# Kernel tuning notes

Hardware: AMD Instinct MI355X
Metric: run time of the kernel (lower is better)

Reference implementation:

```python
import jax, jax.numpy as jnp
import numpy as np

B, S, D = 8, 2048, 1024
NEG = -1000000000.0  # float32 masking constant from original code


def setup_inputs() -> dict:
    key = jax.random.key(0)
    kq, kk, kv, km = jax.random.split(key, 4)
    q = jax.random.normal(kq, (B, S, D), dtype=jnp.float32)
    k = jax.random.normal(kk, (B, S, D), dtype=jnp.float32)
    v = jax.random.normal(kv, (B, S, D), dtype=jnp.float32)
    mask = (jax.random.uniform(km, (B, 1, S)) < 0.1).astype(jnp.float32)
    return {"q": q, "k": k, "v": v, "mask": mask}


def reference(q, k, v, mask):
    scale = jnp.asarray(D ** -0.5, dtype=q.dtype)
    # [B,S,S] = q @ k^T, scaled
    logits = jnp.einsum("bqd,bkd->bqk", q, k) * scale
    logits = logits + mask * NEG  # mask broadcasts over query axis
    attn = jax.nn.softmax(logits, axis=-1)
    return jnp.einsum("bqk,bkd->bqd", attn, v)
```

## Files before the change

### kernel.cpp

```cpp
#include <hip/hip_runtime.h>
#include <hip/hip_bf16.h>

#define NB 8
#define SS 2048
#define DDIM 1024

typedef __attribute__((ext_vector_type(8))) short bf16x8;
typedef __attribute__((ext_vector_type(4))) float f32x4;

__device__ inline void gload_lds16(const void* g, void* l) {
  __builtin_amdgcn_global_load_lds(
      (const __attribute__((address_space(1))) void*)g,
      (__attribute__((address_space(3))) void*)l, 16, 0, 0);
}

__device__ inline ushort f2bf(float f) {
  union { float f; unsigned int u; } v;
  v.f = f;
  unsigned int u = v.u;
  unsigned int r = (u + 0x7FFFu + ((u >> 16) & 1u)) >> 16;
  return (ushort)r;
}

__device__ inline unsigned int pack2(float a, float b) {
  return (unsigned int)f2bf(a) | ((unsigned int)f2bf(b) << 16);
}

__global__ void init_zero(float* __restrict__ p, int n) {
  int i = blockIdx.x * 256 + threadIdx.x;
  if (i < n) p[i] = 0.f;
}

__global__ void conv_bf16(const float* __restrict__ in, ushort* __restrict__ out,
                          int n8) {
  int i = blockIdx.x * 256 + threadIdx.x;
  if (i >= n8) return;
  const float4* p = (const float4*)in + (size_t)i * 2;
  float4 a = p[0], b = p[1];
  uint4 o;
  o.x = pack2(a.x, a.y);
  o.y = pack2(a.z, a.w);
  o.z = pack2(b.x, b.y);
  o.w = pack2(b.z, b.w);
  ((uint4*)out)[i] = o;
}

__global__ void conv_transpose_v(const float* __restrict__ V,
                                 ushort* __restrict__ VT) {
  __shared__ ushort tile[64][65];
  const int b = blockIdx.z;
  const int k0 = blockIdx.x * 64;
  const int d0 = blockIdx.y * 64;
  const float* Vb = V + (size_t)b * SS * DDIM;
  ushort* VTb = VT + (size_t)b * DDIM * SS;
  const int t = threadIdx.x;
#pragma unroll
  for (int i = 0; i < 16; i++) {
    int flat = i * 256 + t;
    int r = flat >> 6, c = flat & 63;
    tile[r][c] = f2bf(Vb[(size_t)(k0 + r) * DDIM + d0 + c]);
  }
  __syncthreads();
#pragma unroll
  for (int i = 0; i < 16; i++) {
    int flat = i * 256 + t;
    int r = flat >> 6, c = flat & 63;
    VTb[(size_t)(d0 + r) * SS + k0 + c] = tile[c][r];
  }
}

template <bool EXPEPI, typename OutT>
__global__ void gemm_bt(const ushort* __restrict__ A, const ushort* __restrict__ Bm,
                        OutT* __restrict__ C, const float* __restrict__ maskp,
                        float* __restrict__ rowsum, int M, int N, int K,
                        float alpha) {
  __shared__ ushort lA[128 * 32];
  __shared__ ushort lB[128 * 32];
  const int tid = threadIdx.x;
  const int wave = tid >> 6, lane = tid & 63;
  const int quad = lane >> 4, l16 = lane & 15;
  const int wm = wave >> 1, wn = wave & 1;
  const int b = blockIdx.z;
  const ushort* Ab = A + (size_t)b * M * K;
  const ushort* Bb = Bm + (size_t)b * N * K;
  const int tileM = blockIdx.y * 128, tileN = blockIdx.x * 128;

  f32x4 acc[4][4];
#pragma unroll
  for (int i = 0; i < 4; i++)
#pragma unroll
    for (int j = 0; j < 4; j++) acc[i][j] = (f32x4){0.f, 0.f, 0.f, 0.f};

  for (int k0 = 0; k0 < K; k0 += 32) {
#pragma unroll
    for (int c = 0; c < 2; c++) {
      int flat = (wave * 2 + c) * 1024 + lane * 16;
      int row = flat >> 6, kb = flat & 63;
      gload_lds16((const char*)Ab + ((size_t)(tileM + row) * K + k0) * 2 + kb,
                  (char*)lA + flat);
      gload_lds16((const char*)Bb + ((size_t)(tileN + row) * K + k0) * 2 + kb,
                  (char*)lB + flat);
    }
    asm volatile("s_waitcnt vmcnt(0)" ::: "memory");
    __syncthreads();

    bf16x8 af[4], bfr[4];
#pragma unroll
    for (int mi = 0; mi < 4; mi++)
      af[mi] = *(const bf16x8*)((const char*)lA +
                                ((wm * 64 + mi * 16 + l16) * 32 + quad * 8) * 2);
#pragma unroll
    for (int ni = 0; ni < 4; ni++)
      bfr[ni] = *(const bf16x8*)((const char*)lB +
                                 ((wn * 64 + ni * 16 + l16) * 32 + quad * 8) * 2);
#pragma unroll
    for (int mi = 0; mi < 4; mi++)
#pragma unroll
      for (int ni = 0; ni < 4; ni++)
        acc[mi][ni] = __builtin_amdgcn_mfma_f32_16x16x32_bf16(af[mi], bfr[ni],
                                                              acc[mi][ni], 0, 0, 0);
    __syncthreads();
  }

  OutT* Cb = C + (size_t)b * M * N;
  if (EXPEPI) {
    const float* mb = maskp + (size_t)b * N;
    float mv[4];
#pragma unroll
    for (int ni = 0; ni < 4; ni++)
      mv[ni] = mb[tileN + wn * 64 + ni * 16 + l16] * (-1e9f);
#pragma unroll
    for (int mi = 0; mi < 4; mi++) {
#pragma unroll
      for (int r = 0; r < 4; r++) {
        int row = tileM + wm * 64 + mi * 16 + quad * 4 + r;
        float s = 0.f;
#pragma unroll
        for (int ni = 0; ni < 4; ni++) {
          int col = tileN + wn * 64 + ni * 16 + l16;
          float e = __expf(acc[mi][ni][r] * alpha + mv[ni]);
          ((ushort*)Cb)[(size_t)row * N + col] = f2bf(e);
          s += e;
        }
        s += __shfl_xor(s, 1, 64);
        s += __shfl_xor(s, 2, 64);
        s += __shfl_xor(s, 4, 64);
        s += __shfl_xor(s, 8, 64);
        if (l16 == 0) atomicAdd(&rowsum[(size_t)b * M + row], s);
      }
    }
  } else {
#pragma unroll
    for (int mi = 0; mi < 4; mi++) {
      float inv[4];
#pragma unroll
      for (int r = 0; r < 4; r++) {
        int row = tileM + wm * 64 + mi * 16 + quad * 4 + r;
        inv[r] = 1.0f / rowsum[(size_t)b * M + row];
      }
#pragma unroll
      for (int ni = 0; ni < 4; ni++) {
        int col = tileN + wn * 64 + ni * 16 + l16;
#pragma unroll
        for (int r = 0; r < 4; r++) {
          int row = tileM + wm * 64 + mi * 16 + quad * 4 + r;
          ((float*)Cb)[(size_t)row * N + col] = acc[mi][ni][r] * alpha * inv[r];
        }
      }
    }
  }
}

extern "C" void kernel_launch(void* const* d_in, const int* in_sizes, int n_in,
                              void* d_out, int out_size, void* d_ws, size_t ws_size,
                              hipStream_t stream) {
  const float* q = (const float*)d_in[0];
  const float* k = (const float*)d_in[1];
  const float* v = (const float*)d_in[2];
  const float* mask = (const float*)d_in[3];
  float* out = (float*)d_out;

  const size_t pQ = (size_t)SS * DDIM * 2;
  const size_t pP = (size_t)SS * SS * 2;
  const size_t pR = (size_t)SS * 4;

  int gb = 8;
  while (gb > 1 && (size_t)gb * (3 * pQ + pP + pR) > ws_size) gb >>= 1;

  for (int b0 = 0; b0 < NB; b0 += gb) {
    char* w = (char*)d_ws;
    ushort* qb = (ushort*)w;
    ushort* kb = (ushort*)(w + (size_t)gb * pQ);
    ushort* vtb = (ushort*)(w + (size_t)gb * pQ * 2);
    ushort* Sc = (ushort*)(w + (size_t)gb * pQ * 3);
    float* rowsum = (float*)(w + (size_t)gb * (pQ * 3 + pP));

    const float* qg = q + (size_t)b0 * SS * DDIM;
    const float* kg = k + (size_t)b0 * SS * DDIM;
    const float* vg = v + (size_t)b0 * SS * DDIM;
    const float* mg = mask + (size_t)b0 * SS;
    float* og = out + (size_t)b0 * SS * DDIM;

    const int nrs = gb * SS;
    init_zero<<<(nrs + 255) / 256, 256, 0, stream>>>(rowsum, nrs);
    const int n8 = gb * SS * DDIM / 8;
    conv_bf16<<<n8 / 256, 256, 0, stream>>>(qg, qb, n8);
    conv_bf16<<<n8 / 256, 256, 0, stream>>>(kg, kb, n8);
    conv_transpose_v<<<dim3(SS / 64, DDIM / 64, gb), 256, 0, stream>>>(vg, vtb);
    gemm_bt<true, ushort><<<dim3(SS / 128, SS / 128, gb), 256, 0, stream>>>(
        qb, kb, Sc, mg, rowsum, SS, SS, DDIM, 0.03125f);
    gemm_bt<false, float><<<dim3(DDIM / 128, SS / 128, gb), 256, 0, stream>>>(
        Sc, vtb, og, nullptr, rowsum, SS, DDIM, SS, 1.0f);
  }
}
```

Measured before the change: 412.0 us.

## Double-buffer GEMM K-loop with swizzled LDS, XCD remap, and vectorized conversions

```diff
diff --git a/kernel.cpp b/kernel.cpp
--- a/kernel.cpp
+++ b/kernel.cpp
@@ -31,10 +31,14 @@
   if (i < n) p[i] = 0.f;
 }
 
-__global__ void conv_bf16(const float* __restrict__ in, ushort* __restrict__ out,
-                          int n8) {
+__global__ void conv_bf16_qk(const float* __restrict__ qin,
+                             const float* __restrict__ kin,
+                             ushort* __restrict__ qout,
+                             ushort* __restrict__ kout, int n8) {
   int i = blockIdx.x * 256 + threadIdx.x;
   if (i >= n8) return;
+  const float* in = blockIdx.y ? kin : qin;
+  ushort* out = blockIdx.y ? kout : qout;
   const float4* p = (const float4*)in + (size_t)i * 2;
   float4 a = p[0], b = p[1];
   uint4 o;
@@ -55,71 +59,145 @@
   ushort* VTb = VT + (size_t)b * DDIM * SS;
   const int t = threadIdx.x;
 #pragma unroll
-  for (int i = 0; i < 16; i++) {
-    int flat = i * 256 + t;
-    int r = flat >> 6, c = flat & 63;
-    tile[r][c] = f2bf(Vb[(size_t)(k0 + r) * DDIM + d0 + c]);
+  for (int i = 0; i < 4; i++) {
+    int j = i * 256 + t;
+    int r = j >> 4, cg = j & 15;
+    float4 f = *(const float4*)(Vb + (size_t)(k0 + r) * DDIM + d0 + cg * 4);
+    tile[r][cg * 4 + 0] = f2bf(f.x);
+    tile[r][cg * 4 + 1] = f2bf(f.y);
+    tile[r][cg * 4 + 2] = f2bf(f.z);
+    tile[r][cg * 4 + 3] = f2bf(f.w);
   }
   __syncthreads();
 #pragma unroll
-  for (int i = 0; i < 16; i++) {
-    int flat = i * 256 + t;
-    int r = flat >> 6, c = flat & 63;
-    VTb[(size_t)(d0 + r) * SS + k0 + c] = tile[c][r];
-  }
-}
+  for (int i = 0; i < 2; i++) {
+    int j = i * 256 + t;
+    int r = j >> 3, cg = j & 7;
+    ushort u[8];
+#pragma unroll
+    for (int u8 = 0; u8 < 8; u8++) u[u8] = tile[cg * 8 + u8][r];
+    *(uint4*)(VTb + (size_t)(d0 + r) * SS + k0 + cg * 8) = *(uint4*)u;
+  }
+}
+
+#define MFMA32()                                                              \
+  _Pragma("unroll") for (int ks = 0; ks < 2; ks++)                            \
+  _Pragma("unroll") for (int mi = 0; mi < 4; mi++)                            \
+  _Pragma("unroll") for (int ni = 0; ni < 4; ni++)                            \
+      acc[mi][ni] = __builtin_amdgcn_mfma_f32_16x16x32_bf16(                  \
+          af[mi][ks], bf[ni][ks], acc[mi][ni], 0, 0, 0);
+
+#define VMW(n) asm volatile("s_waitcnt vmcnt(" #n ")" ::: "memory")
+
+#define RD_A(d)                                                               \
+  _Pragma("unroll") for (int mi = 0; mi < 4; mi++) {                          \
+    const char* _p = ldsc + (d) * 32768 + aoff[mi];                           \
+    af[mi][0] = *(const bf16x8*)(_p + koff0);                                 \
+    af[mi][1] = *(const bf16x8*)(_p + koff1);                                 \
+  }
+
+#define RD_B(d)                                                               \
+  _Pragma("unroll") for (int ni = 0; ni < 4; ni++) {                          \
+    const char* _p = ldsc + (d) * 32768 + 16384 + boff[ni];                   \
+    bf[ni][0] = *(const bf16x8*)(_p + koff0);                                 \
+    bf[ni][1] = *(const bf16x8*)(_p + koff1);                                 \
+  }
+
+#define STAGE(dbuf, kt_)                                                      \
+  do {                                                                        \
+    const ushort* _pa = pA + (size_t)(kt_) * 64;                              \
+    const ushort* _pb = pB + (size_t)(kt_) * 64;                              \
+    char* _la = ldsc + (dbuf) * 32768;                                        \
+    char* _lb = _la + 16384;                                                  \
+    gload_lds16(_pa, _la + olb);                                              \
+    gload_lds16(_pa + 8 * K, _la + olb + 1024);                               \
+    gload_lds16(_pa + 16 * K, _la + olb + 2048);                              \
+    gload_lds16(_pa + 24 * K, _la + olb + 3072);                              \
+    gload_lds16(_pb, _lb + olb);                                              \
+    gload_lds16(_pb + 8 * K, _lb + olb + 1024);                               \
+    gload_lds16(_pb + 16 * K, _lb + olb + 2048);                              \
+    gload_lds16(_pb + 24 * K, _lb + olb + 3072);                              \
+  } while (0)
 
 template <bool EXPEPI, typename OutT>
-__global__ void gemm_bt(const ushort* __restrict__ A, const ushort* __restrict__ Bm,
-                        OutT* __restrict__ C, const float* __restrict__ maskp,
-                        float* __restrict__ rowsum, int M, int N, int K,
-                        float alpha) {
-  __shared__ ushort lA[128 * 32];
-  __shared__ ushort lB[128 * 32];
+__global__ __launch_bounds__(256, 2) void gemm_bt(
+    const ushort* __restrict__ A, const ushort* __restrict__ Bm,
+    OutT* __restrict__ C, const float* __restrict__ maskp,
+    float* __restrict__ rowsum, int M, int N, int K, float alpha) {
+  __shared__ __attribute__((aligned(128))) char ldsc[65536];
   const int tid = threadIdx.x;
   const int wave = tid >> 6, lane = tid & 63;
   const int quad = lane >> 4, l16 = lane & 15;
   const int wm = wave >> 1, wn = wave & 1;
-  const int b = blockIdx.z;
+
+  const int gx = gridDim.x, gy = gridDim.y;
+  const int lin = blockIdx.x + gx * (blockIdx.y + gy * blockIdx.z);
+  const int nwg = gx * gy * (int)gridDim.z;
+  const int cpx = nwg >> 3;
+  const int swz = (lin & 7) * cpx + (lin >> 3);
+  const int bz = swz / (gx * gy);
+  const int rem = swz - bz * (gx * gy);
+  const int by = rem / gx;
+  const int bx = rem - by * gx;
+
+  const int b = bz;
   const ushort* Ab = A + (size_t)b * M * K;
   const ushort* Bb = Bm + (size_t)b * N * K;
-  const int tileM = blockIdx.y * 128, tileN = blockIdx.x * 128;
+  const int tileM = by * 128, tileN = bx * 128;
+
+  const int olb = wave * 4096 + lane * 16;
+  const int r0 = wave * 32 + (lane >> 3);
+  const int c8 = (((lane & 7) ^ (r0 & 7)) * 8);
+  const ushort* __restrict__ pA = Ab + (size_t)(tileM + r0) * K + c8;
+  const ushort* __restrict__ pB = Bb + (size_t)(tileN + r0) * K + c8;
+
+  const int x7 = lane & 7;
+  const int koff0 = ((quad) ^ x7) * 16;
+  const int koff1 = ((4 + quad) ^ x7) * 16;
+  int aoff[4], boff[4];
+#pragma unroll
+  for (int mi = 0; mi < 4; mi++) aoff[mi] = (wm * 64 + mi * 16 + l16) * 128;
+#pragma unroll
+  for (int ni = 0; ni < 4; ni++) boff[ni] = (wn * 64 + ni * 16 + l16) * 128;
 
   f32x4 acc[4][4];
 #pragma unroll
-  for (int i = 0; i < 4; i++)
-#pragma unroll
-    for (int j = 0; j < 4; j++) acc[i][j] = (f32x4){0.f, 0.f, 0.f, 0.f};
-
-  for (int k0 = 0; k0 < K; k0 += 32) {
-#pragma unroll
-    for (int c = 0; c < 2; c++) {
-      int flat = (wave * 2 + c) * 1024 + lane * 16;
-      int row = flat >> 6, kb = flat & 63;
-      gload_lds16((const char*)Ab + ((size_t)(tileM + row) * K + k0) * 2 + kb,
-                  (char*)lA + flat);
-      gload_lds16((const char*)Bb + ((size_t)(tileN + row) * K + k0) * 2 + kb,
-                  (char*)lB + flat);
-    }
-    asm volatile("s_waitcnt vmcnt(0)" ::: "memory");
-    __syncthreads();
-
-    bf16x8 af[4], bfr[4];
-#pragma unroll
-    for (int mi = 0; mi < 4; mi++)
-      af[mi] = *(const bf16x8*)((const char*)lA +
-                                ((wm * 64 + mi * 16 + l16) * 32 + quad * 8) * 2);
-#pragma unroll
-    for (int ni = 0; ni < 4; ni++)
-      bfr[ni] = *(const bf16x8*)((const char*)lB +
-                                 ((wn * 64 + ni * 16 + l16) * 32 + quad * 8) * 2);
-#pragma unroll
-    for (int mi = 0; mi < 4; mi++)
-#pragma unroll
-      for (int ni = 0; ni < 4; ni++)
-        acc[mi][ni] = __builtin_amdgcn_mfma_f32_16x16x32_bf16(af[mi], bfr[ni],
-                                                              acc[mi][ni], 0, 0, 0);
-    __syncthreads();
+  for (int mi = 0; mi < 4; mi++)
+#pragma unroll
+    for (int ni = 0; ni < 4; ni++) acc[mi][ni] = (f32x4){0.f, 0.f, 0.f, 0.f};
+
+  bf16x8 af[4][2], bf[4][2];
+  const int NKT = K >> 6;
+
+  STAGE(0, 0);
+
+  for (int kt = 0; kt < NKT - 1; ++kt) {
+    const int d = kt & 1, dn = d ^ 1;
+    STAGE(dn, kt + 1);
+    VMW(8);
+    __builtin_amdgcn_s_barrier();
+    RD_A(d);
+    RD_B(d);
+    asm volatile("s_waitcnt lgkmcnt(0)" ::: "memory");
+    __builtin_amdgcn_sched_barrier(0);
+    __builtin_amdgcn_s_setprio(1);
+    MFMA32();
+    __builtin_amdgcn_s_setprio(0);
+    __builtin_amdgcn_sched_barrier(0);
+    __builtin_amdgcn_s_barrier();
+  }
+  {
+    const int d = (NKT - 1) & 1;
+    VMW(0);
+    __builtin_amdgcn_s_barrier();
+    RD_A(d);
+    RD_B(d);
+    asm volatile("s_waitcnt lgkmcnt(0)" ::: "memory");
+    __builtin_amdgcn_sched_barrier(0);
+    __builtin_amdgcn_s_setprio(1);
+    MFMA32();
+    __builtin_amdgcn_s_setprio(0);
+    __builtin_amdgcn_sched_barrier(0);
   }
 
   OutT* Cb = C + (size_t)b * M * N;
@@ -132,13 +210,13 @@
 #pragma unroll
     for (int mi = 0; mi < 4; mi++) {
 #pragma unroll
-      for (int r = 0; r < 4; r++) {
-        int row = tileM + wm * 64 + mi * 16 + quad * 4 + r;
+      for (int rr = 0; rr < 4; rr++) {
+        const int row = tileM + wm * 64 + mi * 16 + quad * 4 + rr;
         float s = 0.f;
 #pragma unroll
         for (int ni = 0; ni < 4; ni++) {
-          int col = tileN + wn * 64 + ni * 16 + l16;
-          float e = __expf(acc[mi][ni][r] * alpha + mv[ni]);
+          const int col = tileN + wn * 64 + ni * 16 + l16;
+          float e = __expf(acc[mi][ni][rr] * alpha + mv[ni]);
           ((ushort*)Cb)[(size_t)row * N + col] = f2bf(e);
           s += e;
         }
@@ -154,17 +232,17 @@
     for (int mi = 0; mi < 4; mi++) {
       float inv[4];
 #pragma unroll
-      for (int r = 0; r < 4; r++) {
-        int row = tileM + wm * 64 + mi * 16 + quad * 4 + r;
-        inv[r] = 1.0f / rowsum[(size_t)b * M + row];
+      for (int rr = 0; rr < 4; rr++) {
+        const int row = tileM + wm * 64 + mi * 16 + quad * 4 + rr;
+        inv[rr] = 1.0f / rowsum[(size_t)b * M + row];
       }
 #pragma unroll
       for (int ni = 0; ni < 4; ni++) {
-        int col = tileN + wn * 64 + ni * 16 + l16;
-#pragma unroll
-        for (int r = 0; r < 4; r++) {
-          int row = tileM + wm * 64 + mi * 16 + quad * 4 + r;
-          ((float*)Cb)[(size_t)row * N + col] = acc[mi][ni][r] * alpha * inv[r];
+        const int col = tileN + wn * 64 + ni * 16 + l16;
+#pragma unroll
+        for (int rr = 0; rr < 4; rr++) {
+          const int row = tileM + wm * 64 + mi * 16 + quad * 4 + rr;
+          ((float*)Cb)[(size_t)row * N + col] = acc[mi][ni][rr] * alpha * inv[rr];
         }
       }
     }
@@ -204,8 +282,7 @@
     const int nrs = gb * SS;
     init_zero<<<(nrs + 255) / 256, 256, 0, stream>>>(rowsum, nrs);
     const int n8 = gb * SS * DDIM / 8;
-    conv_bf16<<<n8 / 256, 256, 0, stream>>>(qg, qb, n8);
-    conv_bf16<<<n8 / 256, 256, 0, stream>>>(kg, kb, n8);
+    conv_bf16_qk<<<dim3(n8 / 256, 2), 256, 0, stream>>>(qg, kg, qb, kb, n8);
     conv_transpose_v<<<dim3(SS / 64, DDIM / 64, gb), 256, 0, stream>>>(vg, vtb);
     gemm_bt<true, ushort><<<dim3(SS / 128, SS / 128, gb), 256, 0, stream>>>(
         qb, kb, Sc, mg, rowsum, SS, SS, DDIM, 0.03125f);
```

New measurement: 377.8 us. 1.09x faster.
